# Kernel optimization log

Measured on AMD Instinct MI355X. Metric: run time of the kernel, lower is better.

Reference implementation:

```python
import jax, jax.numpy as jnp
import numpy as np

# ---- config constants (from init_kwargs) ----
NA = 2            # num anchors
NT = 5            # num consecutive frames
NDET = 2          # num_classes + 1
NREG = 6
X_MIN, X_MAX = 0.0, 64.0
Y_MIN, Y_MAX = -32.0, 32.0
CONF_THR = 0.7
ANCHORS = np.array([[3.9, 1.6], [1.0, 0.6]], dtype=np.float32)  # (a_l, a_w)


def setup_inputs() -> dict:
    key = jax.random.key(0)
    k1, k2 = jax.random.split(key)
    nB, nH, nW = 8, 320, 320
    out_detection = jax.random.normal(k1, (nB, NA * NDET * NT, nH, nW), dtype=jnp.float32)
    out_regression = jax.random.normal(k2, (nB, NA * NREG * NT, nH, nW), dtype=jnp.float32)
    return {"out_detection": out_detection, "out_regression": out_regression}


def reference(out_detection, out_regression):
    nB, _, nH, nW = out_detection.shape
    fov_h = X_MAX - X_MIN
    fov_w = Y_MAX - Y_MIN

    # (nB, nA, C, nT, nH, nW) -> (nB, nT, nA, nH, nW, C)
    det = out_detection.reshape(nB, NA, NDET, NT, nH, nW).transpose(0, 3, 1, 4, 5, 2)
    det = jax.nn.softmax(det, axis=-1)
    reg = out_regression.reshape(nB, NA, NREG, NT, nH, nW).transpose(0, 3, 1, 4, 5, 2)

    t_x = jax.nn.sigmoid(reg[..., 0]) * (fov_h / nH)
    t_y = jax.nn.sigmoid(reg[..., 1]) * (fov_w / nW)
    angle = jnp.arctan2(reg[..., 5], reg[..., 4])

    # grids replicate torch's repeat+view memory reinterpretation exactly
    grid_x = (jnp.tile(jnp.arange(nH, dtype=jnp.float32), nW)
              * (fov_h / nH)).reshape(1, 1, 1, nH, nW)
    grid_y = (jnp.tile(jnp.arange(-nW / 2, nW / 2, dtype=jnp.float32), nH)
              * (fov_w / nW)).reshape(1, 1, 1, nH, nW)

    anchors = jnp.asarray(ANCHORS)
    a_l = anchors[:, 0].reshape(1, 1, NA, 1, 1)
    a_w = anchors[:, 1].reshape(1, 1, NA, 1, 1)

    # torch fills reg_boxes from .data (detached); indices 2/3 swap t_l/t_w sources
    reg_boxes = jnp.stack([
        t_x + grid_x,                      # x
        t_y + grid_y,                      # y
        jnp.exp(reg[..., 3]) * a_l,        # l (from t_l = reg[...,3])
        jnp.exp(reg[..., 2]) * a_w,        # w (from t_w = reg[...,2])
        angle,                             # heading
    ], axis=-1)
    reg_boxes = jax.lax.stop_gradient(reg_boxes)

    object_prob = det[..., 1]  # (nB, nT, nA, nH, nW)
    best_anchor = jnp.argmax(object_prob, axis=2)  # max over anchor dim
    mask = (object_prob > CONF_THR) & (
        jnp.arange(NA).reshape(1, 1, NA, 1, 1) == best_anchor[:, :, None]
    )

    # Fixed-shape equivalent of the variable-length compaction: full (box, score)
    # tensor + boolean keep-mask; torch output == boxes_scores[mask] per (b, t).
    boxes_scores = jnp.concatenate([reg_boxes, object_prob[..., None]], axis=-1)
    return boxes_scores, mask
```

## Files before the change

### kernel.cpp

```cpp
#include <hip/hip_runtime.h>
#include <math.h>

constexpr int kNB   = 8;
constexpr int kNT   = 5;
constexpr int kNA   = 2;
constexpr int kNDET = 2;
constexpr int kNREG = 6;
constexpr int kNH   = 320;
constexpr int kNW   = 320;
constexpr int kHW   = kNH * kNW;
constexpr int kHW4  = kHW / 4;
constexpr int kDetCh = kNA * kNDET * kNT;
constexpr int kRegCh = kNA * kNREG * kNT;
constexpr int kBoxFloats = kNB * kNT * kNA * kHW * 6;
constexpr int kQuads = kNB * kNT * kHW4;

__device__ __forceinline__ float sigmoidf_(float x) {
    return 1.0f / (1.0f + expf(-x));
}

__global__ __launch_bounds__(256) void fafe_predict(
    const float* __restrict__ det, const float* __restrict__ reg,
    float* __restrict__ out)
{
    const int idx = blockIdx.x * blockDim.x + threadIdx.x;
    if (idx >= kQuads) return;

    const int q  = idx % kHW4;
    const int bt = idx / kHW4;
    const int t  = bt % kNT;
    const int b  = bt / kNT;
    const int s  = q * 4;
    const int wb = s % kNW;

    const float4* det4 = reinterpret_cast<const float4*>(det);
    const float4* reg4 = reinterpret_cast<const float4*>(reg);
    float4* out4 = reinterpret_cast<float4*>(out);

    constexpr int kPlane6o4  = kHW * 6 / 4;
    constexpr int kMaskBase4 = kBoxFloats / 4;

    const int dbase = (b * kDetCh + t) * kHW4 + q;
    const float4 d00 = det4[dbase + 0 * kHW4];
    const float4 d01 = det4[dbase + 5 * kHW4];
    const float4 d10 = det4[dbase + 10 * kHW4];
    const float4 d11 = det4[dbase + 15 * kHW4];

    float p0[4], p1[4];
    float4 m0v, m1v;
    {
        const float* x00 = reinterpret_cast<const float*>(&d00);
        const float* x01 = reinterpret_cast<const float*>(&d01);
        const float* x10 = reinterpret_cast<const float*>(&d10);
        const float* x11 = reinterpret_cast<const float*>(&d11);
        float* pm0 = reinterpret_cast<float*>(&m0v);
        float* pm1 = reinterpret_cast<float*>(&m1v);
#pragma unroll
        for (int j = 0; j < 4; ++j) {
            p0[j] = sigmoidf_(x01[j] - x00[j]);
            p1[j] = sigmoidf_(x11[j] - x10[j]);
            const bool best1 = p1[j] > p0[j];
            pm0[j] = (p0[j] > 0.7f && !best1) ? 1.0f : 0.0f;
            pm1[j] = (p1[j] > 0.7f && best1) ? 1.0f : 0.0f;
        }
    }
    out4[kMaskBase4 + (bt * 2 + 0) * kHW4 + q] = m0v;
    out4[kMaskBase4 + (bt * 2 + 1) * kHW4 + q] = m1v;

    const int rbase = (b * kRegCh + t) * kHW4 + q;
#pragma unroll
    for (int a = 0; a < kNA; ++a) {
        const int ab = rbase + a * 30 * kHW4;
        const float4 r0 = reg4[ab + 0 * kHW4];
        const float4 r1 = reg4[ab + 5 * kHW4];
        const float4 r2 = reg4[ab + 10 * kHW4];
        const float4 r3 = reg4[ab + 15 * kHW4];
        const float4 r4 = reg4[ab + 20 * kHW4];
        const float4 r5 = reg4[ab + 25 * kHW4];

        const float a_l = (a == 0) ? 3.9f : 1.0f;
        const float a_w = (a == 0) ? 1.6f : 0.6f;
        const float* pp = (a == 0) ? p0 : p1;

        const float* x0 = reinterpret_cast<const float*>(&r0);
        const float* x1 = reinterpret_cast<const float*>(&r1);
        const float* x2 = reinterpret_cast<const float*>(&r2);
        const float* x3 = reinterpret_cast<const float*>(&r3);
        const float* x4 = reinterpret_cast<const float*>(&r4);
        const float* x5 = reinterpret_cast<const float*>(&r5);

        alignas(16) float boxes[24];
#pragma unroll
        for (int j = 0; j < 4; ++j) {
            const float gw  = (float)(wb + j);
            const float gwm = gw - 160.0f;
            boxes[j*6 + 0] = sigmoidf_(x0[j]) * 0.2f + gw  * 0.2f;
            boxes[j*6 + 1] = sigmoidf_(x1[j]) * 0.2f + gwm * 0.2f;
            boxes[j*6 + 2] = expf(x3[j]) * a_l;
            boxes[j*6 + 3] = expf(x2[j]) * a_w;
            boxes[j*6 + 4] = atan2f(x5[j], x4[j]);
            boxes[j*6 + 5] = pp[j];
        }

        const int ob = (bt * 2 + a) * kPlane6o4 + q * 6;
        const float4* bv = reinterpret_cast<const float4*>(boxes);
#pragma unroll
        for (int m = 0; m < 6; ++m) out4[ob + m] = bv[m];
    }
}

extern "C" void kernel_launch(void* const* d_in, const int* in_sizes, int n_in,
                              void* d_out, int out_size, void* d_ws, size_t ws_size,
                              hipStream_t stream) {
    const float* det = (const float*)d_in[0];
    const float* reg = (const float*)d_in[1];
    float* out = (float*)d_out;

    constexpr int kBlock = 256;
    constexpr int kGrid = (kQuads + kBlock - 1) / kBlock;
    fafe_predict<<<kGrid, kBlock, 0, stream>>>(det, reg, out);
}
```

Before: 433.7 us.

## Stage box outputs through LDS for coalesced stores; use nontemporal writes

Each thread's box results are written to shared memory component by component, then read back interleaved so that consecutive threads store consecutive float4s of the AoS output, replacing the per-thread 6 strided float4 stores. All output stores also become nontemporal. This targets store coalescing and cache pollution on a write-heavy kernel, at the cost of LDS traffic, possible bank conflicts from the stride-1024 gather, and two block barriers per anchor.

```diff
diff --git a/kernel.cpp b/kernel.cpp
--- a/kernel.cpp
+++ b/kernel.cpp
@@ -14,6 +14,10 @@
 constexpr int kRegCh = kNA * kNREG * kNT;
 constexpr int kBoxFloats = kNB * kNT * kNA * kHW * 6;
 constexpr int kQuads = kNB * kNT * kHW4;
+constexpr int kBlock = 256;
+constexpr int kGrid  = kQuads / kBlock;
+
+typedef float f32x4 __attribute__((ext_vector_type(4)));
 
 __device__ __forceinline__ float sigmoidf_(float x) {
     return 1.0f / (1.0f + expf(-x));
@@ -23,15 +27,17 @@
     const float* __restrict__ det, const float* __restrict__ reg,
     float* __restrict__ out)
 {
-    const int idx = blockIdx.x * blockDim.x + threadIdx.x;
-    if (idx >= kQuads) return;
+    __shared__ f32x4 lds4[6 * 256];
+    float* ldsf = reinterpret_cast<float*>(lds4);
 
-    const int q  = idx % kHW4;
-    const int bt = idx / kHW4;
-    const int t  = bt % kNT;
-    const int b  = bt / kNT;
-    const int s  = q * 4;
-    const int wb = s % kNW;
+    const int tid = threadIdx.x;
+    const int idx = blockIdx.x * kBlock + tid;
+    const int q   = idx % kHW4;
+    const int bt  = idx / kHW4;
+    const int t   = bt % kNT;
+    const int b   = bt / kNT;
+    const int wb  = (q * 4) % kNW;
+    const int qbase = q - tid;
 
     const float4* det4 = reinterpret_cast<const float4*>(det);
     const float4* reg4 = reinterpret_cast<const float4*>(reg);
@@ -41,38 +47,38 @@
     constexpr int kMaskBase4 = kBoxFloats / 4;
 
     const int dbase = (b * kDetCh + t) * kHW4 + q;
-    const float4 d00 = det4[dbase + 0 * kHW4];
-    const float4 d01 = det4[dbase + 5 * kHW4];
+    const float4 d00 = det4[dbase + 0  * kHW4];
+    const float4 d01 = det4[dbase + 5  * kHW4];
     const float4 d10 = det4[dbase + 10 * kHW4];
     const float4 d11 = det4[dbase + 15 * kHW4];
 
     float p0[4], p1[4];
-    float4 m0v, m1v;
+    f32x4 m0v, m1v;
     {
         const float* x00 = reinterpret_cast<const float*>(&d00);
         const float* x01 = reinterpret_cast<const float*>(&d01);
         const float* x10 = reinterpret_cast<const float*>(&d10);
         const float* x11 = reinterpret_cast<const float*>(&d11);
-        float* pm0 = reinterpret_cast<float*>(&m0v);
-        float* pm1 = reinterpret_cast<float*>(&m1v);
 #pragma unroll
         for (int j = 0; j < 4; ++j) {
             p0[j] = sigmoidf_(x01[j] - x00[j]);
             p1[j] = sigmoidf_(x11[j] - x10[j]);
             const bool best1 = p1[j] > p0[j];
-            pm0[j] = (p0[j] > 0.7f && !best1) ? 1.0f : 0.0f;
-            pm1[j] = (p1[j] > 0.7f && best1) ? 1.0f : 0.0f;
+            m0v[j] = (p0[j] > 0.7f && !best1) ? 1.0f : 0.0f;
+            m1v[j] = (p1[j] > 0.7f && best1) ? 1.0f : 0.0f;
         }
     }
-    out4[kMaskBase4 + (bt * 2 + 0) * kHW4 + q] = m0v;
-    out4[kMaskBase4 + (bt * 2 + 1) * kHW4 + q] = m1v;
+    __builtin_nontemporal_store(
+        m0v, reinterpret_cast<f32x4*>(&out4[kMaskBase4 + (bt * 2 + 0) * kHW4 + q]));
+    __builtin_nontemporal_store(
+        m1v, reinterpret_cast<f32x4*>(&out4[kMaskBase4 + (bt * 2 + 1) * kHW4 + q]));
 
     const int rbase = (b * kRegCh + t) * kHW4 + q;
 #pragma unroll
     for (int a = 0; a < kNA; ++a) {
         const int ab = rbase + a * 30 * kHW4;
-        const float4 r0 = reg4[ab + 0 * kHW4];
-        const float4 r1 = reg4[ab + 5 * kHW4];
+        const float4 r0 = reg4[ab + 0  * kHW4];
+        const float4 r1 = reg4[ab + 5  * kHW4];
         const float4 r2 = reg4[ab + 10 * kHW4];
         const float4 r3 = reg4[ab + 15 * kHW4];
         const float4 r4 = reg4[ab + 20 * kHW4];
@@ -89,23 +95,42 @@
         const float* x4 = reinterpret_cast<const float*>(&r4);
         const float* x5 = reinterpret_cast<const float*>(&r5);
 
-        alignas(16) float boxes[24];
+        f32x4 cx, cy, cl, cw, cg, cs;
 #pragma unroll
         for (int j = 0; j < 4; ++j) {
             const float gw  = (float)(wb + j);
             const float gwm = gw - 160.0f;
-            boxes[j*6 + 0] = sigmoidf_(x0[j]) * 0.2f + gw  * 0.2f;
-            boxes[j*6 + 1] = sigmoidf_(x1[j]) * 0.2f + gwm * 0.2f;
-            boxes[j*6 + 2] = expf(x3[j]) * a_l;
-            boxes[j*6 + 3] = expf(x2[j]) * a_w;
-            boxes[j*6 + 4] = atan2f(x5[j], x4[j]);
-            boxes[j*6 + 5] = pp[j];
+            cx[j] = sigmoidf_(x0[j]) * 0.2f + gw  * 0.2f;
+            cy[j] = sigmoidf_(x1[j]) * 0.2f + gwm * 0.2f;
+            cl[j] = expf(x3[j]) * a_l;
+            cw[j] = expf(x2[j]) * a_w;
+            cg[j] = atan2f(x5[j], x4[j]);
+            cs[j] = pp[j];
         }
 
-        const int ob = (bt * 2 + a) * kPlane6o4 + q * 6;
-        const float4* bv = reinterpret_cast<const float4*>(boxes);
+        if (a == 1) __syncthreads();
+        lds4[0 * 256 + tid] = cx;
+        lds4[1 * 256 + tid] = cy;
+        lds4[2 * 256 + tid] = cl;
+        lds4[3 * 256 + tid] = cw;
+        lds4[4 * 256 + tid] = cg;
+        lds4[5 * 256 + tid] = cs;
+        __syncthreads();
+
+        const int obase = (bt * 2 + a) * kPlane6o4 + qbase * 6;
 #pragma unroll
-        for (int m = 0; m < 6; ++m) out4[ob + m] = bv[m];
+        for (int k = 0; k < 6; ++k) {
+            const int o  = k * 256 + tid;
+            const int f0 = 4 * o;
+            f32x4 v;
+#pragma unroll
+            for (int e = 0; e < 4; ++e) {
+                const int f = f0 + e;
+                v[e] = ldsf[(f % 6) * 1024 + (f / 6)];
+            }
+            __builtin_nontemporal_store(
+                v, reinterpret_cast<f32x4*>(&out4[obase + o]));
+        }
     }
 }
 
@@ -115,8 +140,5 @@
     const float* det = (const float*)d_in[0];
     const float* reg = (const float*)d_in[1];
     float* out = (float*)d_out;
-
-    constexpr int kBlock = 256;
-    constexpr int kGrid = (kQuads + kBlock - 1) / kBlock;
     fafe_predict<<<kGrid, kBlock, 0, stream>>>(det, reg, out);
 }
```

Result: faster. 406.1 us (-6.4%).
